# Optimization experiments

Hardware: AMD Instinct MI355X
Metric: run time of the kernel (lower is better)

Reference implementation:

```python
import jax, jax.numpy as jnp
import numpy as np

NUM_POINTS = 1024  # K from init_kwargs


def setup_inputs() -> dict:
    key = jax.random.key(0)
    # [B, N, C]: xyz in channels 0:3, extra features (e.g. normals) in 3:6
    points = jax.random.normal(key, (16, 131072, 6), dtype=jnp.float32)
    return {"points": points}


def _fps_indices(xyz, K):
    """Iterative farthest-point sampling. xyz: [B, N, 3] -> idx [B, K] int32.
    random_start_point in the torch source is replaced by a fixed start (index 0)
    for determinism; the algorithm is otherwise identical."""
    B, N, _ = xyz.shape
    start = jnp.zeros((B,), dtype=jnp.int32)
    init_dists = jnp.full((B, N), jnp.inf, dtype=xyz.dtype)

    def step(carry, _):
        dists, last = carry
        # gather last selected point: [B, 1, 3]
        p = jnp.take_along_axis(xyz, last[:, None, None], axis=1)
        d = jnp.sum((xyz - p) ** 2, axis=-1)          # [B, N]
        dists = jnp.minimum(dists, d)                 # running min dist to selected set
        nxt = jnp.argmax(dists, axis=-1).astype(jnp.int32)
        return (dists, nxt), nxt

    (_, _), rest = jax.lax.scan(step, (init_dists, start), None, length=K - 1)
    # rest: [K-1, B] -> assemble [B, K] with the start index first
    idx = jnp.concatenate([start[:, None], rest.T], axis=1)
    return idx


def reference(points):
    xyz = points[:, :, :3].astype(jnp.float32)
    idx = _fps_indices(xyz, NUM_POINTS)               # [B, K]
    # masked_gather (all indices valid): gather rows along point dim
    out = jnp.take_along_axis(points, idx[:, :, None], axis=1)  # [B, K, C]
    return out
```

## Files before the change

### kernel.cpp

```cpp
#include <hip/hip_runtime.h>

#define BATCH 16
#define NPTS  131072
#define NCH   6
#define KSEL  1024
#define MBLK  16
#define TPB   256
#define CHUNK (NPTS / MBLK)
#define PPT   (CHUNK / TPB)
#define ROT   2


extern "C" __global__ __launch_bounds__(TPB)
__attribute__((amdgpu_waves_per_eu(2, 2)))
void fps_kernel(const float* __restrict__ pts, float* __restrict__ out,
                unsigned long long* __restrict__ pub)
{
#pragma clang fp contract(off)
    __shared__ float              s_wd[TPB / 64];
    __shared__ int                s_wi[TPB / 64];
    __shared__ unsigned long long s_key[MBLK];

    const int b    = blockIdx.x / MBLK;
    const int m    = blockIdx.x % MBLK;
    const int tid  = threadIdx.x;
    const int base = m * CHUNK;
    const float* __restrict__ pb = pts + (size_t)b * NPTS * NCH;

    float xr[PPT], yr[PPT], zr[PPT], dmin[PPT];
#pragma unroll
    for (int i = 0; i < PPT; ++i) {
        const float* p = pb + (size_t)(base + tid + i * TPB) * NCH;
        xr[i]   = p[0];
        yr[i]   = p[1];
        zr[i]   = p[2];
        dmin[i] = __builtin_inff();
    }
#pragma unroll
    for (int i = 0; i < PPT; ++i) {
        asm volatile("" : "+v"(xr[i]), "+v"(yr[i]), "+v"(zr[i]));
    }

    if (m == 0 && tid < NCH) out[(size_t)b * KSEL * NCH + tid] = pb[tid];

    float px = pb[0], py = pb[1], pz = pb[2];

    for (int k = 1; k < KSEL; ++k) {
        float bd = -1.0f;
        int   bj = 0;
#pragma unroll
        for (int i = 0; i < PPT; ++i) {
            float dx = __fsub_rn(xr[i], px);
            float dy = __fsub_rn(yr[i], py);
            float dz = __fsub_rn(zr[i], pz);
            float d  = __fadd_rn(__fadd_rn(__fmul_rn(dx, dx),
                                           __fmul_rn(dy, dy)),
                                 __fmul_rn(dz, dz));
            float dm = dmin[i];
            dm = (d < dm) ? d : dm;
            dmin[i] = dm;
            if (dm > bd) { bd = dm; bj = tid + i * TPB; }
        }

        for (int off = 32; off > 0; off >>= 1) {
            float od = __shfl_down(bd, off);
            int   oj = __shfl_down(bj, off);
            if (od > bd || (od == bd && oj < bj)) { bd = od; bj = oj; }
        }
        if ((tid & 63) == 0) {
            const int w = tid >> 6;
            s_wd[w] = bd; s_wi[w] = bj;
        }
        __syncthreads();

        unsigned long long* slot =
            pub + ((size_t)b * ROT + (size_t)(k & (ROT - 1))) * MBLK;

        if (tid == 0) {
            float fd = s_wd[0]; int fi = s_wi[0];
#pragma unroll
            for (int w = 1; w < TPB / 64; ++w) {
                if (s_wd[w] > fd || (s_wd[w] == fd && s_wi[w] < fi)) {
                    fd = s_wd[w]; fi = s_wi[w];
                }
            }
            const unsigned g   = (unsigned)(base + fi);
            const unsigned inv = 0xFFFFFu ^ g;
            unsigned long long key =
                ((unsigned long long)__float_as_uint(fd) << 32)
                | ((unsigned long long)inv << 12)
                | (unsigned long long)(unsigned)k;
            __hip_atomic_store(&slot[m], key, __ATOMIC_RELAXED,
                               __HIP_MEMORY_SCOPE_AGENT);
        }

        if (tid < MBLK) {
            unsigned long long v;
            do {
                v = __hip_atomic_load(&slot[tid], __ATOMIC_RELAXED,
                                      __HIP_MEMORY_SCOPE_AGENT);
            } while ((unsigned)(v & 0xFFFull) != (unsigned)k);
            s_key[tid] = v;
        }
        __syncthreads();

        unsigned long long mx = s_key[0];
#pragma unroll
        for (int w = 1; w < MBLK; ++w) {
            if (s_key[w] > mx) mx = s_key[w];
        }
        const unsigned g = 0xFFFFFu ^ (unsigned)((mx >> 12) & 0xFFFFFull);
        const float* pp = pb + (size_t)g * NCH;
        px = pp[0]; py = pp[1]; pz = pp[2];

        if ((k & (MBLK - 1)) == m && tid == 0) {
            float* o = out + ((size_t)b * KSEL + k) * NCH;
#pragma unroll
            for (int c = 0; c < NCH; ++c) o[c] = pp[c];
        }
    }
}

extern "C" void kernel_launch(void* const* d_in, const int* in_sizes, int n_in,
                              void* d_out, int out_size, void* d_ws, size_t ws_size,
                              hipStream_t stream) {
    const float* pts = (const float*)d_in[0];
    float* out = (float*)d_out;
    unsigned long long* pub = (unsigned long long*)d_ws;

    hipMemsetAsync(d_ws, 0,
                   (size_t)BATCH * ROT * MBLK * sizeof(unsigned long long),
                   stream);

    void* args[] = { (void*)&pts, (void*)&out, (void*)&pub };
    hipLaunchCooperativeKernel((const void*)fps_kernel,
                               dim3(BATCH * MBLK), dim3(TPB),
                               args, 0, stream);
}
```

Measured before the change: 2.898 ms.

## Move per-thread xyz from registers to LDS and interleave batch block mapping

Stores each block's chunk of x, y, z coordinates in dynamic shared memory (96 KB per block) instead of keeping them in registers, and drops the waves-per-EU attribute. The aim is to ease register pressure so the compiler can schedule more freely. It also remaps block indices so consecutive blocks belong to different batches, which may change how blocks spread across compute units. In exchange, every iteration now issues three LDS reads per point, adding LDS bandwidth and latency to the hot loop.

```diff
diff --git a/kernel.cpp b/kernel.cpp
--- a/kernel.cpp
+++ b/kernel.cpp
@@ -9,36 +9,37 @@
 #define CHUNK (NPTS / MBLK)
 #define PPT   (CHUNK / TPB)
 #define ROT   2
+#define LDSB  (3 * CHUNK * 4)
 
 
 extern "C" __global__ __launch_bounds__(TPB)
-__attribute__((amdgpu_waves_per_eu(2, 2)))
 void fps_kernel(const float* __restrict__ pts, float* __restrict__ out,
                 unsigned long long* __restrict__ pub)
 {
 #pragma clang fp contract(off)
+    extern __shared__ float sm[];
+    float* sx = sm;
+    float* sy = sm + CHUNK;
+    float* sz = sm + 2 * CHUNK;
     __shared__ float              s_wd[TPB / 64];
     __shared__ int                s_wi[TPB / 64];
     __shared__ unsigned long long s_key[MBLK];
 
-    const int b    = blockIdx.x / MBLK;
-    const int m    = blockIdx.x % MBLK;
+    const int b    = blockIdx.x % BATCH;
+    const int m    = blockIdx.x / BATCH;
     const int tid  = threadIdx.x;
     const int base = m * CHUNK;
     const float* __restrict__ pb = pts + (size_t)b * NPTS * NCH;
 
-    float xr[PPT], yr[PPT], zr[PPT], dmin[PPT];
+    float dmin[PPT];
 #pragma unroll
     for (int i = 0; i < PPT; ++i) {
-        const float* p = pb + (size_t)(base + tid + i * TPB) * NCH;
-        xr[i]   = p[0];
-        yr[i]   = p[1];
-        zr[i]   = p[2];
+        const int idx = tid + i * TPB;
+        const float* p = pb + (size_t)(base + idx) * NCH;
+        sx[idx] = p[0];
+        sy[idx] = p[1];
+        sz[idx] = p[2];
         dmin[i] = __builtin_inff();
-    }
-#pragma unroll
-    for (int i = 0; i < PPT; ++i) {
-        asm volatile("" : "+v"(xr[i]), "+v"(yr[i]), "+v"(zr[i]));
     }
 
     if (m == 0 && tid < NCH) out[(size_t)b * KSEL * NCH + tid] = pb[tid];
@@ -50,16 +51,17 @@
         int   bj = 0;
 #pragma unroll
         for (int i = 0; i < PPT; ++i) {
-            float dx = __fsub_rn(xr[i], px);
-            float dy = __fsub_rn(yr[i], py);
-            float dz = __fsub_rn(zr[i], pz);
+            const int idx = tid + i * TPB;
+            float dx = __fsub_rn(sx[idx], px);
+            float dy = __fsub_rn(sy[idx], py);
+            float dz = __fsub_rn(sz[idx], pz);
             float d  = __fadd_rn(__fadd_rn(__fmul_rn(dx, dx),
                                            __fmul_rn(dy, dy)),
                                  __fmul_rn(dz, dz));
             float dm = dmin[i];
             dm = (d < dm) ? d : dm;
             dmin[i] = dm;
-            if (dm > bd) { bd = dm; bj = tid + i * TPB; }
+            if (dm > bd) { bd = dm; bj = idx; }
         }
 
         for (int off = 32; off > 0; off >>= 1) {
@@ -135,5 +137,5 @@
     void* args[] = { (void*)&pts, (void*)&out, (void*)&pub };
     hipLaunchCooperativeKernel((const void*)fps_kernel,
                                dim3(BATCH * MBLK), dim3(TPB),
-                               args, 0, stream);
+                               args, LDSB, stream);
 }
```

After: 3.259 ms. 12.5% more time.
